# Performance work log

Hardware: AMD Instinct MI355X
Metric: run time of the kernel (lower is better)

The kernel has to match this reference:

```python
import jax, jax.numpy as jnp
import numpy as np

N_NODES = 300000
N_EDGES = 1200000
D = 128
B = 1000
VOCAB = 26  # vocab_size + 1


def setup_inputs() -> dict:
    key = jax.random.key(0)
    ks = jax.random.split(key, 10)
    x = jax.random.randint(ks[0], (N_NODES,), 0, VOCAB, dtype=jnp.int32)
    edge_index = jax.random.randint(ks[1], (2, N_EDGES), 0, N_NODES, dtype=jnp.int32)
    # cumulative protein boundaries: B proteins of equal length, last entry == N_NODES
    amino_acids_numbers = (jnp.arange(1, B + 1, dtype=jnp.int32) * (N_NODES // B))
    s = 1.0 / np.sqrt(D)
    emb = jax.random.normal(ks[2], (VOCAB, D), dtype=jnp.float32)
    W_rel1 = jax.random.uniform(ks[3], (D, D), jnp.float32, -s, s)
    b_rel1 = jax.random.uniform(ks[4], (D,), jnp.float32, -s, s)
    W_root1 = jax.random.uniform(ks[5], (D, D), jnp.float32, -s, s)
    W_rel2 = jax.random.uniform(ks[6], (D, D), jnp.float32, -s, s)
    b_rel2 = jax.random.uniform(ks[7], (D,), jnp.float32, -s, s)
    W_root2 = jax.random.uniform(ks[8], (D, D), jnp.float32, -s, s)
    return {"x": x, "edge_index": edge_index, "amino_acids_numbers": amino_acids_numbers,
            "emb": emb, "W_rel1": W_rel1, "b_rel1": b_rel1, "W_root1": W_root1,
            "W_rel2": W_rel2, "b_rel2": b_rel2, "W_root2": W_root2}


def _graph_conv(nodes, src, tgt, W_rel, b_rel, W_root, n):
    # PyG GraphConv (aggr='add'): out = Lin_rel(sum_{j->i} x_j) + Lin_root(x_i)
    agg = jax.ops.segment_sum(nodes[src], tgt, num_segments=n)  # [N, D]
    return agg @ W_rel.T + b_rel + nodes @ W_root.T


def reference(x, edge_index, amino_acids_numbers, emb,
              W_rel1, b_rel1, W_root1, W_rel2, b_rel2, W_root2):
    n = x.shape[0]
    src, tgt = edge_index[0], edge_index[1]
    nodes = emb[x]  # [N, D] embedding lookup
    nodes = _graph_conv(nodes, src, tgt, W_rel1, b_rel1, W_root1, n)
    nodes = _graph_conv(nodes, src, tgt, W_rel2, b_rel2, W_root2, n)
    # segment mean pooling over [start:end) slices defined by cumulative ends
    ends = amino_acids_numbers
    seg = jnp.searchsorted(ends, jnp.arange(n), side='right')  # node -> protein id
    b = ends.shape[0]
    sums = jax.ops.segment_sum(nodes, seg, num_segments=b)  # [B, D]
    counts = jnp.diff(ends, prepend=jnp.zeros((1,), ends.dtype)).astype(nodes.dtype)
    return sums / counts[:, None]
```

## Files before the change

kernel.cpp:

```cpp
#include <hip/hip_runtime.h>

#define DD 128
#define VV 26
#define NW 13
#define CS8 8
#define NB 256
#define TWIN 512

__device__ __forceinline__ unsigned wsum(unsigned v) {
#pragma unroll
    for (int m = 32; m >= 1; m >>= 1) v += __shfl_xor(v, m, 64);
    return v;
}

__device__ __forceinline__ int seg_guess(const int* ends, int B, int t, int Lavg) {
    int p = t / Lavg;
    if (p > B - 1) p = B - 1;
    while (p > 0 && ends[p - 1] > t) --p;
    while (ends[p] <= t) ++p;
    return p;
}

__device__ __forceinline__ int bseg(const int* cumx, int j) {
    int lo = 0, hi = NB - 1;
    while (lo < hi) {
        int mid = (lo + hi + 1) >> 1;
        if (cumx[mid] <= j) lo = mid; else hi = mid - 1;
    }
    return lo;
}

__global__ __launch_bounds__(1024)
void k_sort_pre(const int* __restrict__ src, const int* __restrict__ tgt,
                const int* __restrict__ x, const int* __restrict__ ends,
                int E, int B, int chunk, int chunkp, int Lavg,
                const float* __restrict__ emb,
                const float* __restrict__ W1r, const float* __restrict__ b1,
                const float* __restrict__ W1o,
                const float* __restrict__ W2r, const float* __restrict__ W2o,
                unsigned short* __restrict__ sorted_tl, unsigned* __restrict__ sorted_s,
                int* __restrict__ segstart, int* __restrict__ seghist,
                float* __restrict__ P1, float* __restrict__ P2,
                float* __restrict__ P3, float* __restrict__ uvec,
                float* __restrict__ wvec) {
    extern __shared__ int lds[];
    int tid = threadIdx.x;

    if (blockIdx.x >= NB) {
        float* e1r = (float*)lds;
        float* r1r = e1r + DD;
        float* b1s = r1r + DD;
        int v = blockIdx.x - NB;
        int d = tid;
        if (d < DD) {
            const float* e = emb + v * DD;
            const float* w1r = W1r + d * DD;
            const float* w1o = W1o + d * DD;
            float s1 = 0.f, s2 = 0.f;
            for (int k = 0; k < DD; ++k) {
                float ev = e[k];
                s1 += ev * w1r[k];
                s2 += ev * w1o[k];
            }
            e1r[d] = s1; r1r[d] = s2; b1s[d] = b1[d];
        }
        __syncthreads();
        if (d < DD) {
            const float* wr = W2r + d * DD;
            const float* wo = W2o + d * DD;
            float p1 = 0.f, p2 = 0.f, p3 = 0.f, su = 0.f, sw = 0.f;
            for (int k = 0; k < DD; ++k) {
                float a = wr[k], b = wo[k], ee = e1r[k], r = r1r[k], bb = b1s[k];
                p1 += ee * a; p2 += r * a + ee * b; p3 += r * b;
                su += bb * a; sw += bb * b;
            }
            P1[v * DD + d] = p1; P2[v * DD + d] = p2; P3[v * DD + d] = p3;
            if (v == 0) { uvec[d] = su; wvec[d] = sw; }
        }
        return;
    }

    int* lds_ends = lds;
    int* scan     = lds + B;
    int* cur      = scan + 1024;
    unsigned short* lpe = (unsigned short*)(cur + B);
    unsigned short* stl = lpe + chunkp;
    unsigned* sts = (unsigned*)(stl + chunkp);

    int b = blockIdx.x;
    int e0 = b * chunk;
    int e1 = min(E, e0 + chunk);
    int clen = e1 - e0;

    for (int i = tid; i < B; i += 1024) lds_ends[i] = ends[i];
    scan[tid] = 0;
    __syncthreads();

    for (int i = tid; i < clen; i += 1024) {
        int t = tgt[e0 + i];
        int p = seg_guess(lds_ends, B, t, Lavg);
        atomicAdd(&scan[p], 1);
        lpe[i] = (unsigned short)p;
    }
    __syncthreads();
    int v = scan[tid];
    if (tid < B) seghist[b * B + tid] = v;
    for (int off = 1; off < 1024; off <<= 1) {
        int t = (tid >= off) ? scan[tid - off] : 0;
        __syncthreads();
        scan[tid] += t;
        __syncthreads();
    }
    if (tid < B) {
        int excl = scan[tid] - v;
        cur[tid] = excl;
        segstart[b * B + tid] = e0 + excl;
    }
    __syncthreads();

    for (int i = tid; i < clen; i += 1024) {
        int e = e0 + i;
        int p = lpe[i];
        int s = src[e];
        int t = tgt[e];
        int lbl = x[s];
        int pst = (p == 0) ? 0 : lds_ends[p - 1];
        int pos = atomicAdd(&cur[p], 1);
        stl[pos] = (unsigned short)(((t - pst) << 5) | lbl);
        sts[pos] = (unsigned)s;
    }
    __syncthreads();

    for (int i = tid; i < clen; i += 1024) {
        sorted_tl[e0 + i] = stl[i];
        sorted_s[e0 + i] = sts[i];
    }
}

__global__ __launch_bounds__(256)
void k_counts(const int* __restrict__ x, const int* __restrict__ ends,
              const int* __restrict__ segstart, const int* __restrict__ seghist,
              int B, int E, const unsigned short* __restrict__ sorted_tl,
              unsigned* __restrict__ counts,
              float* __restrict__ CpG, float* __restrict__ HpG) {
    __shared__ unsigned tab[TWIN * CS8];
    __shared__ int sc[NB], cumx[NB + 1], segb[NB];
    __shared__ unsigned red[4][2 * NW];
    int p = blockIdx.x, tid = threadIdx.x;
    int start = (p == 0) ? 0 : ends[p - 1];
    int end = ends[p];
    int Lp = end - start;

    int h = seghist[tid * B + p];
    segb[tid] = segstart[tid * B + p];
    sc[tid] = h;
    __syncthreads();
    for (int off = 1; off < NB; off <<= 1) {
        int t = (tid >= off) ? sc[tid - off] : 0;
        __syncthreads();
        sc[tid] += t;
        __syncthreads();
    }
    cumx[tid] = sc[tid] - h;
    if (tid == NB - 1) cumx[NB] = sc[NB - 1];
    __syncthreads();
    int Dp = cumx[NB];

    unsigned cpw[NW], hpw[NW];
#pragma unroll
    for (int w = 0; w < NW; ++w) { cpw[w] = 0u; hpw[w] = 0u; }

    for (int i = start + tid; i < end; i += 256) {
        int l = x[i];
        unsigned inc = 1u << ((l & 1) * 16);
        int wi = l >> 1;
#pragma unroll
        for (int w = 0; w < NW; ++w) hpw[w] += (w == wi) ? inc : 0u;
    }

    for (int w0 = 0; w0 < Lp; w0 += TWIN) {
        int wlen = min(TWIN, Lp - w0);
        __syncthreads();
        for (int i = tid; i < wlen * CS8; i += 256) tab[i] = 0u;
        __syncthreads();
        for (int j = tid; j < Dp; j += 256) {
            int bb = bseg(cumx, j);
            int pos = segb[bb] + (j - cumx[bb]);
            unsigned tl = (unsigned)sorted_tl[pos];
            int lbl = (int)(tl & 31u);
            int tloc = (int)(tl >> 5) - w0;
            if ((unsigned)tloc < (unsigned)wlen)
                atomicAdd(&tab[tloc * CS8 + (lbl >> 2)], 1u << ((lbl & 3) * 8));
            if (w0 == 0) {
                unsigned inc = 1u << ((lbl & 1) * 16);
                int wi = lbl >> 1;
#pragma unroll
                for (int w = 0; w < NW; ++w) cpw[w] += (w == wi) ? inc : 0u;
            }
        }
        __syncthreads();
        for (int idx = tid; idx < wlen * CS8; idx += 256) {
            int r = idx >> 3, w = idx & 7;
            counts[((size_t)(start + w0 + r)) * CS8 + w] = tab[r * CS8 + w];
        }
    }

    int wave = tid >> 6, lane = tid & 63;
#pragma unroll
    for (int w = 0; w < NW; ++w) {
        unsigned a = wsum(cpw[w]); if (lane == 0) red[wave][w] = a;
        unsigned b = wsum(hpw[w]); if (lane == 0) red[wave][NW + w] = b;
    }
    __syncthreads();
    if (tid < 2 * NW) {
        unsigned t = red[0][tid] + red[1][tid] + red[2][tid] + red[3][tid];
        int grp = tid / NW, w = tid % NW;
        float* dst = (grp == 0) ? (CpG + (size_t)p * VV) : (HpG + (size_t)p * VV);
        dst[w * 2] = (float)(t & 0xFFFFu);
        if (w * 2 + 1 < VV) dst[w * 2 + 1] = (float)(t >> 16);
    }
}

__global__ __launch_bounds__(256)
void k_protein(const int* __restrict__ ends,
               const int* __restrict__ segstart, const int* __restrict__ seghist,
               const unsigned* __restrict__ sorted_s,
               const unsigned* __restrict__ counts,
               const float* __restrict__ CpG, const float* __restrict__ HpG,
               const float* __restrict__ P1, const float* __restrict__ P2,
               const float* __restrict__ P3, const float* __restrict__ uvec,
               const float* __restrict__ wvec, const float* __restrict__ b2,
               int B, int E, float* __restrict__ out) {
    __shared__ int sc[NB], cumx[NB + 1], segb[NB];
    __shared__ unsigned red[4][14];
    __shared__ float c2f[VV], cpf[VV], hpf[VV];
    int p = blockIdx.x, tid = threadIdx.x;
    int start = (p == 0) ? 0 : ends[p - 1];
    int end = ends[p];

    int h = seghist[tid * B + p];
    segb[tid] = segstart[tid * B + p];
    sc[tid] = h;
    __syncthreads();
    for (int off = 1; off < NB; off <<= 1) {
        int t = (tid >= off) ? sc[tid - off] : 0;
        __syncthreads();
        sc[tid] += t;
        __syncthreads();
    }
    cumx[tid] = sc[tid] - h;
    if (tid == NB - 1) cumx[NB] = sc[NB - 1];
    __syncthreads();
    int Dp = cumx[NB];

    unsigned ua[7], ub[7];
#pragma unroll
    for (int k = 0; k < 7; ++k) { ua[k] = 0u; ub[k] = 0u; }
    for (int j = tid; j < Dp; j += 256) {
        int bb = bseg(cumx, j);
        int pos = segb[bb] + (j - cumx[bb]);
        int s = (int)sorted_s[pos];
        const uint4* cb = reinterpret_cast<const uint4*>(counts + (size_t)s * CS8);
        uint4 c0 = cb[0], c1 = cb[1];
        unsigned w;
        w = c0.x; ua[0] += w & 0x00FF00FFu; ub[0] += (w >> 8) & 0x00FF00FFu;
        w = c0.y; ua[1] += w & 0x00FF00FFu; ub[1] += (w >> 8) & 0x00FF00FFu;
        w = c0.z; ua[2] += w & 0x00FF00FFu; ub[2] += (w >> 8) & 0x00FF00FFu;
        w = c0.w; ua[3] += w & 0x00FF00FFu; ub[3] += (w >> 8) & 0x00FF00FFu;
        w = c1.x; ua[4] += w & 0x00FF00FFu; ub[4] += (w >> 8) & 0x00FF00FFu;
        w = c1.y; ua[5] += w & 0x00FF00FFu; ub[5] += (w >> 8) & 0x00FF00FFu;
        w = c1.z; ua[6] += w & 0x00FF00FFu; ub[6] += (w >> 8) & 0x00FF00FFu;
    }

    int wave = tid >> 6, lane = tid & 63;
#pragma unroll
    for (int k = 0; k < 7; ++k) {
        unsigned a = wsum(ua[k]); if (lane == 0) red[wave][2 * k] = a;
        unsigned b = wsum(ub[k]); if (lane == 0) red[wave][2 * k + 1] = b;
    }
    if (tid >= 64 && tid < 64 + VV)   cpf[tid - 64]  = CpG[(size_t)p * VV + (tid - 64)];
    if (tid >= 128 && tid < 128 + VV) hpf[tid - 128] = HpG[(size_t)p * VV + (tid - 128)];
    __syncthreads();
    if (tid < 14) {
        unsigned t = red[0][tid] + red[1][tid] + red[2][tid] + red[3][tid];
        int k = tid >> 1, isB = tid & 1;
        int base = 4 * k + isB;
        c2f[base] = (float)(t & 0xFFFFu);
        if (base + 2 < VV) c2f[base + 2] = (float)(t >> 16);
    }
    __syncthreads();

    if (tid < DD) {
        int d = tid;
        float acc = 0.f;
#pragma unroll
        for (int v = 0; v < VV; ++v)
            acc += c2f[v] * P1[v * DD + d] + cpf[v] * P2[v * DD + d] + hpf[v] * P3[v * DD + d];
        float Lp = (float)(end - start);
        float invL = 1.f / Lp;
        float Dpf = (float)Dp;
        out[(size_t)p * DD + d] = acc * invL + (Dpf * invL) * uvec[d] + wvec[d] + b2[d];
    }
}

extern "C" void kernel_launch(void* const* d_in, const int* in_sizes, int n_in,
                              void* d_out, int out_size, void* d_ws, size_t ws_size,
                              hipStream_t stream) {
    const int*   x       = (const int*)d_in[0];
    const int*   edge    = (const int*)d_in[1];
    const int*   ends    = (const int*)d_in[2];
    const float* emb     = (const float*)d_in[3];
    const float* W_rel1  = (const float*)d_in[4];
    const float* b_rel1  = (const float*)d_in[5];
    const float* W_root1 = (const float*)d_in[6];
    const float* W_rel2  = (const float*)d_in[7];
    const float* b_rel2  = (const float*)d_in[8];
    const float* W_root2 = (const float*)d_in[9];

    const int N = in_sizes[0];
    const int E = in_sizes[1] / 2;
    const int B = in_sizes[2];
    const int Lavg = (N / B) > 0 ? (N / B) : 1;
    const int chunk = (E + NB - 1) / NB;
    const int chunkp = (chunk + 1) & ~1;

    const int* srcp = edge;
    const int* tgtp = edge + E;

    auto align256 = [](size_t v) { return (v + 255) & ~(size_t)255; };
    char* ws = (char*)d_ws;
    size_t off = 0;
    unsigned* counts = (unsigned*)(ws + off);               off += align256((size_t)N * CS8 * 4);
    int* segstart = (int*)(ws + off);                       off += align256((size_t)NB * B * 4);
    int* seghist = (int*)(ws + off);                        off += align256((size_t)NB * B * 4);
    unsigned short* sorted_tl = (unsigned short*)(ws + off); off += align256((size_t)E * 2);
    unsigned* sorted_s = (unsigned*)(ws + off);             off += align256((size_t)E * 4);
    float* CpG = (float*)(ws + off);                        off += align256((size_t)B * VV * 4);
    float* HpG = (float*)(ws + off);                        off += align256((size_t)B * VV * 4);
    float* P1 = (float*)(ws + off);                         off += align256((size_t)VV * DD * 4);
    float* P2 = (float*)(ws + off);                         off += align256((size_t)VV * DD * 4);
    float* P3 = (float*)(ws + off);                         off += align256((size_t)VV * DD * 4);
    float* uvec = (float*)(ws + off);                       off += align256((size_t)DD * 4);
    float* wvec = (float*)(ws + off);                       off += align256((size_t)DD * 4);
    (void)ws_size; (void)n_in; (void)out_size;


    size_t ldsb = (size_t)(B + 1024 + B) * 4 + (size_t)chunkp * 4 + (size_t)chunk * 4;
    k_sort_pre<<<NB + VV, 1024, ldsb, stream>>>(
        srcp, tgtp, x, ends, E, B, chunk, chunkp, Lavg,
        emb, W_rel1, b_rel1, W_root1, W_rel2, W_root2,
        sorted_tl, sorted_s, segstart, seghist, P1, P2, P3, uvec, wvec);

    k_counts<<<B, 256, 0, stream>>>(x, ends, segstart, seghist, B, E, sorted_tl,
                                    counts, CpG, HpG);

    k_protein<<<B, 256, 0, stream>>>(ends, segstart, seghist, sorted_s, counts, CpG, HpG,
                                     P1, P2, P3, uvec, wvec, b_rel2, B, E, (float*)d_out);
}
```

Before: 72.24 us.

## Merge three kernels into one cooperative persistent kernel with grid syncs

Replaces the sort, counts and protein kernels with a single cooperative kernel of 256 blocks of 1024 threads that separates phases with grid.sync. The per-protein prefix scan over chunk histograms is computed once into global buffers (pcum/psegb) and reused by both later phases, where before it was repeated in each kernel. Per-protein work now runs in 1024-thread blocks striding over proteins, so each block handles about four proteins. The aim is to remove launch gaps and redundant scans, at the cost of grid-barrier overhead, fewer resident blocks for the per-protein phases, and the 26 weight-precompute blocks now sitting serially in front of the sort in the first blocks.

```diff
diff --git a/kernel.cpp b/kernel.cpp
--- a/kernel.cpp
+++ b/kernel.cpp
@@ -1,11 +1,16 @@
 #include <hip/hip_runtime.h>
+#include <hip/hip_cooperative_groups.h>
+
+namespace cg = cooperative_groups;
 
 #define DD 128
 #define VV 26
 #define NW 13
 #define CS8 8
-#define NB 256
+#define G 256
+#define T 1024
 #define TWIN 512
+#define PCS 260
 
 __device__ __forceinline__ unsigned wsum(unsigned v) {
 #pragma unroll
@@ -22,7 +27,7 @@
 }
 
 __device__ __forceinline__ int bseg(const int* cumx, int j) {
-    int lo = 0, hi = NB - 1;
+    int lo = 0, hi = G - 1;
     while (lo < hi) {
         int mid = (lo + hi + 1) >> 1;
         if (cumx[mid] <= j) lo = mid; else hi = mid - 1;
@@ -30,38 +35,38 @@
     return lo;
 }
 
-__global__ __launch_bounds__(1024)
-void k_sort_pre(const int* __restrict__ src, const int* __restrict__ tgt,
-                const int* __restrict__ x, const int* __restrict__ ends,
-                int E, int B, int chunk, int chunkp, int Lavg,
-                const float* __restrict__ emb,
-                const float* __restrict__ W1r, const float* __restrict__ b1,
-                const float* __restrict__ W1o,
-                const float* __restrict__ W2r, const float* __restrict__ W2o,
-                unsigned short* __restrict__ sorted_tl, unsigned* __restrict__ sorted_s,
-                int* __restrict__ segstart, int* __restrict__ seghist,
-                float* __restrict__ P1, float* __restrict__ P2,
-                float* __restrict__ P3, float* __restrict__ uvec,
-                float* __restrict__ wvec) {
-    extern __shared__ int lds[];
+__global__ void __launch_bounds__(T, 4)
+k_all(const int* __restrict__ src, const int* __restrict__ tgt,
+      const int* __restrict__ x, const int* __restrict__ ends,
+      int E, int B, int chunk, int Lavg,
+      const float* __restrict__ emb, const float* __restrict__ W1r,
+      const float* __restrict__ b1, const float* __restrict__ W1o,
+      const float* __restrict__ W2r, const float* __restrict__ W2o,
+      int* __restrict__ segstart, int* __restrict__ seghist,
+      unsigned short* __restrict__ sorted_tl, unsigned* __restrict__ sorted_s,
+      int* __restrict__ pcum, int* __restrict__ psegb,
+      unsigned* __restrict__ counts, float* __restrict__ CpG, float* __restrict__ HpG,
+      float* __restrict__ P1, float* __restrict__ P2, float* __restrict__ P3,
+      float* __restrict__ uvec, float* __restrict__ wvec,
+      const float* __restrict__ b2, float* __restrict__ out)
+{
+    extern __shared__ char smem[];
+    cg::grid_group grid = cg::this_grid();
     int tid = threadIdx.x;
-
-    if (blockIdx.x >= NB) {
-        float* e1r = (float*)lds;
+    int blk = blockIdx.x;
+    int chunkp = (chunk + 1) & ~1;
+
+    if (blk < VV) {
+        float* e1r = (float*)smem;
         float* r1r = e1r + DD;
         float* b1s = r1r + DD;
-        int v = blockIdx.x - NB;
-        int d = tid;
+        int v = blk, d = tid;
         if (d < DD) {
             const float* e = emb + v * DD;
             const float* w1r = W1r + d * DD;
             const float* w1o = W1o + d * DD;
             float s1 = 0.f, s2 = 0.f;
-            for (int k = 0; k < DD; ++k) {
-                float ev = e[k];
-                s1 += ev * w1r[k];
-                s2 += ev * w1o[k];
-            }
+            for (int k = 0; k < DD; ++k) { float ev = e[k]; s1 += ev * w1r[k]; s2 += ev * w1o[k]; }
             e1r[d] = s1; r1r[d] = s2; b1s[d] = b1[d];
         }
         __syncthreads();
@@ -70,236 +75,236 @@
             const float* wo = W2o + d * DD;
             float p1 = 0.f, p2 = 0.f, p3 = 0.f, su = 0.f, sw = 0.f;
             for (int k = 0; k < DD; ++k) {
-                float a = wr[k], b = wo[k], ee = e1r[k], r = r1r[k], bb = b1s[k];
-                p1 += ee * a; p2 += r * a + ee * b; p3 += r * b;
-                su += bb * a; sw += bb * b;
+                float a = wr[k], bb = wo[k], ee = e1r[k], r = r1r[k], c = b1s[k];
+                p1 += ee * a; p2 += r * a + ee * bb; p3 += r * bb;
+                su += c * a; sw += c * bb;
             }
             P1[v * DD + d] = p1; P2[v * DD + d] = p2; P3[v * DD + d] = p3;
             if (v == 0) { uvec[d] = su; wvec[d] = sw; }
         }
-        return;
-    }
-
-    int* lds_ends = lds;
-    int* scan     = lds + B;
-    int* cur      = scan + 1024;
-    unsigned short* lpe = (unsigned short*)(cur + B);
-    unsigned short* stl = lpe + chunkp;
-    unsigned* sts = (unsigned*)(stl + chunkp);
-
-    int b = blockIdx.x;
-    int e0 = b * chunk;
-    int e1 = min(E, e0 + chunk);
-    int clen = e1 - e0;
-
-    for (int i = tid; i < B; i += 1024) lds_ends[i] = ends[i];
-    scan[tid] = 0;
-    __syncthreads();
-
-    for (int i = tid; i < clen; i += 1024) {
-        int t = tgt[e0 + i];
-        int p = seg_guess(lds_ends, B, t, Lavg);
-        atomicAdd(&scan[p], 1);
-        lpe[i] = (unsigned short)p;
-    }
-    __syncthreads();
-    int v = scan[tid];
-    if (tid < B) seghist[b * B + tid] = v;
-    for (int off = 1; off < 1024; off <<= 1) {
-        int t = (tid >= off) ? scan[tid - off] : 0;
-        __syncthreads();
-        scan[tid] += t;
-        __syncthreads();
-    }
-    if (tid < B) {
-        int excl = scan[tid] - v;
-        cur[tid] = excl;
-        segstart[b * B + tid] = e0 + excl;
-    }
-    __syncthreads();
-
-    for (int i = tid; i < clen; i += 1024) {
-        int e = e0 + i;
-        int p = lpe[i];
-        int s = src[e];
-        int t = tgt[e];
-        int lbl = x[s];
-        int pst = (p == 0) ? 0 : lds_ends[p - 1];
-        int pos = atomicAdd(&cur[p], 1);
-        stl[pos] = (unsigned short)(((t - pst) << 5) | lbl);
-        sts[pos] = (unsigned)s;
-    }
-    __syncthreads();
-
-    for (int i = tid; i < clen; i += 1024) {
-        sorted_tl[e0 + i] = stl[i];
-        sorted_s[e0 + i] = sts[i];
-    }
-}
-
-__global__ __launch_bounds__(256)
-void k_counts(const int* __restrict__ x, const int* __restrict__ ends,
-              const int* __restrict__ segstart, const int* __restrict__ seghist,
-              int B, int E, const unsigned short* __restrict__ sorted_tl,
-              unsigned* __restrict__ counts,
-              float* __restrict__ CpG, float* __restrict__ HpG) {
-    __shared__ unsigned tab[TWIN * CS8];
-    __shared__ int sc[NB], cumx[NB + 1], segb[NB];
-    __shared__ unsigned red[4][2 * NW];
-    int p = blockIdx.x, tid = threadIdx.x;
-    int start = (p == 0) ? 0 : ends[p - 1];
-    int end = ends[p];
-    int Lp = end - start;
-
-    int h = seghist[tid * B + p];
-    segb[tid] = segstart[tid * B + p];
-    sc[tid] = h;
-    __syncthreads();
-    for (int off = 1; off < NB; off <<= 1) {
-        int t = (tid >= off) ? sc[tid - off] : 0;
-        __syncthreads();
-        sc[tid] += t;
-        __syncthreads();
-    }
-    cumx[tid] = sc[tid] - h;
-    if (tid == NB - 1) cumx[NB] = sc[NB - 1];
-    __syncthreads();
-    int Dp = cumx[NB];
-
-    unsigned cpw[NW], hpw[NW];
-#pragma unroll
-    for (int w = 0; w < NW; ++w) { cpw[w] = 0u; hpw[w] = 0u; }
-
-    for (int i = start + tid; i < end; i += 256) {
-        int l = x[i];
-        unsigned inc = 1u << ((l & 1) * 16);
-        int wi = l >> 1;
-#pragma unroll
-        for (int w = 0; w < NW; ++w) hpw[w] += (w == wi) ? inc : 0u;
-    }
-
-    for (int w0 = 0; w0 < Lp; w0 += TWIN) {
-        int wlen = min(TWIN, Lp - w0);
-        __syncthreads();
-        for (int i = tid; i < wlen * CS8; i += 256) tab[i] = 0u;
-        __syncthreads();
-        for (int j = tid; j < Dp; j += 256) {
-            int bb = bseg(cumx, j);
-            int pos = segb[bb] + (j - cumx[bb]);
-            unsigned tl = (unsigned)sorted_tl[pos];
-            int lbl = (int)(tl & 31u);
-            int tloc = (int)(tl >> 5) - w0;
-            if ((unsigned)tloc < (unsigned)wlen)
-                atomicAdd(&tab[tloc * CS8 + (lbl >> 2)], 1u << ((lbl & 3) * 8));
-            if (w0 == 0) {
-                unsigned inc = 1u << ((lbl & 1) * 16);
-                int wi = lbl >> 1;
-#pragma unroll
-                for (int w = 0; w < NW; ++w) cpw[w] += (w == wi) ? inc : 0u;
-            }
-        }
-        __syncthreads();
-        for (int idx = tid; idx < wlen * CS8; idx += 256) {
-            int r = idx >> 3, w = idx & 7;
-            counts[((size_t)(start + w0 + r)) * CS8 + w] = tab[r * CS8 + w];
-        }
-    }
-
-    int wave = tid >> 6, lane = tid & 63;
-#pragma unroll
-    for (int w = 0; w < NW; ++w) {
-        unsigned a = wsum(cpw[w]); if (lane == 0) red[wave][w] = a;
-        unsigned b = wsum(hpw[w]); if (lane == 0) red[wave][NW + w] = b;
-    }
-    __syncthreads();
-    if (tid < 2 * NW) {
-        unsigned t = red[0][tid] + red[1][tid] + red[2][tid] + red[3][tid];
-        int grp = tid / NW, w = tid % NW;
-        float* dst = (grp == 0) ? (CpG + (size_t)p * VV) : (HpG + (size_t)p * VV);
-        dst[w * 2] = (float)(t & 0xFFFFu);
-        if (w * 2 + 1 < VV) dst[w * 2 + 1] = (float)(t >> 16);
-    }
-}
-
-__global__ __launch_bounds__(256)
-void k_protein(const int* __restrict__ ends,
-               const int* __restrict__ segstart, const int* __restrict__ seghist,
-               const unsigned* __restrict__ sorted_s,
-               const unsigned* __restrict__ counts,
-               const float* __restrict__ CpG, const float* __restrict__ HpG,
-               const float* __restrict__ P1, const float* __restrict__ P2,
-               const float* __restrict__ P3, const float* __restrict__ uvec,
-               const float* __restrict__ wvec, const float* __restrict__ b2,
-               int B, int E, float* __restrict__ out) {
-    __shared__ int sc[NB], cumx[NB + 1], segb[NB];
-    __shared__ unsigned red[4][14];
-    __shared__ float c2f[VV], cpf[VV], hpf[VV];
-    int p = blockIdx.x, tid = threadIdx.x;
-    int start = (p == 0) ? 0 : ends[p - 1];
-    int end = ends[p];
-
-    int h = seghist[tid * B + p];
-    segb[tid] = segstart[tid * B + p];
-    sc[tid] = h;
-    __syncthreads();
-    for (int off = 1; off < NB; off <<= 1) {
-        int t = (tid >= off) ? sc[tid - off] : 0;
-        __syncthreads();
-        sc[tid] += t;
-        __syncthreads();
-    }
-    cumx[tid] = sc[tid] - h;
-    if (tid == NB - 1) cumx[NB] = sc[NB - 1];
-    __syncthreads();
-    int Dp = cumx[NB];
-
-    unsigned ua[7], ub[7];
-#pragma unroll
-    for (int k = 0; k < 7; ++k) { ua[k] = 0u; ub[k] = 0u; }
-    for (int j = tid; j < Dp; j += 256) {
-        int bb = bseg(cumx, j);
-        int pos = segb[bb] + (j - cumx[bb]);
-        int s = (int)sorted_s[pos];
-        const uint4* cb = reinterpret_cast<const uint4*>(counts + (size_t)s * CS8);
-        uint4 c0 = cb[0], c1 = cb[1];
-        unsigned w;
-        w = c0.x; ua[0] += w & 0x00FF00FFu; ub[0] += (w >> 8) & 0x00FF00FFu;
-        w = c0.y; ua[1] += w & 0x00FF00FFu; ub[1] += (w >> 8) & 0x00FF00FFu;
-        w = c0.z; ua[2] += w & 0x00FF00FFu; ub[2] += (w >> 8) & 0x00FF00FFu;
-        w = c0.w; ua[3] += w & 0x00FF00FFu; ub[3] += (w >> 8) & 0x00FF00FFu;
-        w = c1.x; ua[4] += w & 0x00FF00FFu; ub[4] += (w >> 8) & 0x00FF00FFu;
-        w = c1.y; ua[5] += w & 0x00FF00FFu; ub[5] += (w >> 8) & 0x00FF00FFu;
-        w = c1.z; ua[6] += w & 0x00FF00FFu; ub[6] += (w >> 8) & 0x00FF00FFu;
-    }
-
-    int wave = tid >> 6, lane = tid & 63;
-#pragma unroll
-    for (int k = 0; k < 7; ++k) {
-        unsigned a = wsum(ua[k]); if (lane == 0) red[wave][2 * k] = a;
-        unsigned b = wsum(ub[k]); if (lane == 0) red[wave][2 * k + 1] = b;
-    }
-    if (tid >= 64 && tid < 64 + VV)   cpf[tid - 64]  = CpG[(size_t)p * VV + (tid - 64)];
-    if (tid >= 128 && tid < 128 + VV) hpf[tid - 128] = HpG[(size_t)p * VV + (tid - 128)];
-    __syncthreads();
-    if (tid < 14) {
-        unsigned t = red[0][tid] + red[1][tid] + red[2][tid] + red[3][tid];
-        int k = tid >> 1, isB = tid & 1;
-        int base = 4 * k + isB;
-        c2f[base] = (float)(t & 0xFFFFu);
-        if (base + 2 < VV) c2f[base + 2] = (float)(t >> 16);
-    }
-    __syncthreads();
-
-    if (tid < DD) {
-        int d = tid;
-        float acc = 0.f;
-#pragma unroll
-        for (int v = 0; v < VV; ++v)
-            acc += c2f[v] * P1[v * DD + d] + cpf[v] * P2[v * DD + d] + hpf[v] * P3[v * DD + d];
-        float Lp = (float)(end - start);
-        float invL = 1.f / Lp;
-        float Dpf = (float)Dp;
-        out[(size_t)p * DD + d] = acc * invL + (Dpf * invL) * uvec[d] + wvec[d] + b2[d];
+        __syncthreads();
+    }
+
+    {
+        int* lds_ends = (int*)smem;
+        int* scan = lds_ends + 1024;
+        int* cur = scan + 1024;
+        unsigned short* lpe = (unsigned short*)(cur + 1024);
+        unsigned short* stl = lpe + chunkp;
+        unsigned* sts = (unsigned*)(stl + chunkp);
+
+        int e0 = blk * chunk;
+        int e1 = min(E, e0 + chunk);
+        int clen = e1 - e0;
+        for (int i = tid; i < B; i += T) lds_ends[i] = ends[i];
+        scan[tid] = 0;
+        __syncthreads();
+        for (int i = tid; i < clen; i += T) {
+            int t = tgt[e0 + i];
+            int p = seg_guess(lds_ends, B, t, Lavg);
+            atomicAdd(&scan[p], 1);
+            lpe[i] = (unsigned short)p;
+        }
+        __syncthreads();
+        int v = scan[tid];
+        if (tid < B) seghist[blk * B + tid] = v;
+        for (int off = 1; off < T; off <<= 1) {
+            int t = (tid >= off) ? scan[tid - off] : 0;
+            __syncthreads();
+            scan[tid] += t;
+            __syncthreads();
+        }
+        if (tid < B) {
+            int excl = scan[tid] - v;
+            cur[tid] = excl;
+            segstart[blk * B + tid] = e0 + excl;
+        }
+        __syncthreads();
+        for (int i = tid; i < clen; i += T) {
+            int e = e0 + i;
+            int p = lpe[i];
+            int s = src[e];
+            int t = tgt[e];
+            int lbl = x[s];
+            int pst = (p == 0) ? 0 : lds_ends[p - 1];
+            int pos = atomicAdd(&cur[p], 1);
+            stl[pos] = (unsigned short)(((t - pst) << 5) | lbl);
+            sts[pos] = (unsigned)s;
+        }
+        __syncthreads();
+        for (int i = tid; i < clen; i += T) {
+            sorted_tl[e0 + i] = stl[i];
+            sorted_s[e0 + i] = sts[i];
+        }
+    }
+
+    grid.sync();
+
+    {
+        int* h = (int*)smem;
+        for (int p = blk; p < B; p += G) {
+            int v = 0;
+            if (tid < G) { v = seghist[tid * B + p]; h[tid] = v; }
+            __syncthreads();
+            for (int off = 1; off < G; off <<= 1) {
+                int t = (tid >= off && tid < G) ? h[tid - off] : 0;
+                __syncthreads();
+                if (tid < G) h[tid] += t;
+                __syncthreads();
+            }
+            if (tid < G) {
+                pcum[p * PCS + tid] = h[tid] - v;
+                psegb[p * G + tid] = segstart[tid * B + p];
+            }
+            if (tid == G - 1) pcum[p * PCS + G] = h[G - 1];
+            __syncthreads();
+        }
+    }
+
+    grid.sync();
+
+    {
+        unsigned* tab = (unsigned*)smem;
+        int* cumx = (int*)(smem + TWIN * CS8 * 4);
+        int* segb = cumx + 260;
+        unsigned* red = (unsigned*)(segb + 256);
+
+        for (int p = blk; p < B; p += G) {
+            int start = (p == 0) ? 0 : ends[p - 1];
+            int end = ends[p];
+            int Lp = end - start;
+            if (tid <= G) cumx[tid] = pcum[p * PCS + tid];
+            if (tid < G) segb[tid] = psegb[p * G + tid];
+            __syncthreads();
+            int Dp = cumx[G];
+
+            unsigned cpw[NW], hpw[NW];
+#pragma unroll
+            for (int w = 0; w < NW; ++w) { cpw[w] = 0u; hpw[w] = 0u; }
+
+            for (int i = start + tid; i < end; i += T) {
+                int l = x[i];
+                unsigned inc = 1u << ((l & 1) * 16);
+                int wi = l >> 1;
+#pragma unroll
+                for (int w = 0; w < NW; ++w) hpw[w] += (w == wi) ? inc : 0u;
+            }
+
+            for (int w0 = 0; w0 < Lp; w0 += TWIN) {
+                int wlen = min(TWIN, Lp - w0);
+                __syncthreads();
+                for (int i = tid; i < wlen * CS8; i += T) tab[i] = 0u;
+                __syncthreads();
+                for (int j = tid; j < Dp; j += T) {
+                    int bb = bseg(cumx, j);
+                    int pos = segb[bb] + (j - cumx[bb]);
+                    unsigned tl = (unsigned)sorted_tl[pos];
+                    int lbl = (int)(tl & 31u);
+                    int tloc = (int)(tl >> 5) - w0;
+                    if ((unsigned)tloc < (unsigned)wlen)
+                        atomicAdd(&tab[tloc * CS8 + (lbl >> 2)], 1u << ((lbl & 3) * 8));
+                    if (w0 == 0) {
+                        unsigned inc = 1u << ((lbl & 1) * 16);
+                        int wi = lbl >> 1;
+#pragma unroll
+                        for (int w = 0; w < NW; ++w) cpw[w] += (w == wi) ? inc : 0u;
+                    }
+                }
+                __syncthreads();
+                for (int idx = tid; idx < wlen * CS8; idx += T) {
+                    int r = idx >> 3, w = idx & 7;
+                    counts[((size_t)(start + w0 + r)) * CS8 + w] = tab[r * CS8 + w];
+                }
+            }
+
+            int wave = tid >> 6, lane = tid & 63;
+#pragma unroll
+            for (int w = 0; w < NW; ++w) {
+                unsigned a = wsum(cpw[w]); if (lane == 0) red[wave * 26 + w] = a;
+                unsigned b = wsum(hpw[w]); if (lane == 0) red[wave * 26 + NW + w] = b;
+            }
+            __syncthreads();
+            if (tid < 2 * NW) {
+                unsigned t = 0;
+#pragma unroll
+                for (int w = 0; w < 16; ++w) t += red[w * 26 + tid];
+                int grp = tid / NW, w = tid % NW;
+                float* dst = (grp == 0) ? (CpG + (size_t)p * VV) : (HpG + (size_t)p * VV);
+                dst[w * 2] = (float)(t & 0xFFFFu);
+                if (w * 2 + 1 < VV) dst[w * 2 + 1] = (float)(t >> 16);
+            }
+            __syncthreads();
+        }
+    }
+
+    grid.sync();
+
+    {
+        int* cumx = (int*)smem;
+        int* segb = cumx + 260;
+        unsigned* red = (unsigned*)(segb + 256);
+        float* c2f = (float*)(red + 16 * 14);
+        float* cpf = c2f + VV;
+        float* hpf = cpf + VV;
+
+        for (int p = blk; p < B; p += G) {
+            int start = (p == 0) ? 0 : ends[p - 1];
+            int end = ends[p];
+            if (tid <= G) cumx[tid] = pcum[p * PCS + tid];
+            if (tid < G) segb[tid] = psegb[p * G + tid];
+            __syncthreads();
+            int Dp = cumx[G];
+
+            unsigned ua[7], ub[7];
+#pragma unroll
+            for (int k = 0; k < 7; ++k) { ua[k] = 0u; ub[k] = 0u; }
+            for (int j = tid; j < Dp; j += T) {
+                int bb = bseg(cumx, j);
+                int pos = segb[bb] + (j - cumx[bb]);
+                int s = (int)sorted_s[pos];
+                const uint4* cb = reinterpret_cast<const uint4*>(counts + (size_t)s * CS8);
+                uint4 c0 = cb[0], c1 = cb[1];
+                unsigned w;
+                w = c0.x; ua[0] += w & 0x00FF00FFu; ub[0] += (w >> 8) & 0x00FF00FFu;
+                w = c0.y; ua[1] += w & 0x00FF00FFu; ub[1] += (w >> 8) & 0x00FF00FFu;
+                w = c0.z; ua[2] += w & 0x00FF00FFu; ub[2] += (w >> 8) & 0x00FF00FFu;
+                w = c0.w; ua[3] += w & 0x00FF00FFu; ub[3] += (w >> 8) & 0x00FF00FFu;
+                w = c1.x; ua[4] += w & 0x00FF00FFu; ub[4] += (w >> 8) & 0x00FF00FFu;
+                w = c1.y; ua[5] += w & 0x00FF00FFu; ub[5] += (w >> 8) & 0x00FF00FFu;
+                w = c1.z; ua[6] += w & 0x00FF00FFu; ub[6] += (w >> 8) & 0x00FF00FFu;
+            }
+
+            int wave = tid >> 6, lane = tid & 63;
+#pragma unroll
+            for (int k = 0; k < 7; ++k) {
+                unsigned a = wsum(ua[k]); if (lane == 0) red[wave * 14 + 2 * k] = a;
+                unsigned b = wsum(ub[k]); if (lane == 0) red[wave * 14 + 2 * k + 1] = b;
+            }
+            if (tid >= 64 && tid < 64 + VV)   cpf[tid - 64]  = CpG[(size_t)p * VV + (tid - 64)];
+            if (tid >= 128 && tid < 128 + VV) hpf[tid - 128] = HpG[(size_t)p * VV + (tid - 128)];
+            __syncthreads();
+            if (tid < 14) {
+                unsigned t = 0;
+#pragma unroll
+                for (int w = 0; w < 16; ++w) t += red[w * 14 + tid];
+                int k = tid >> 1, isB = tid & 1;
+                int base = 4 * k + isB;
+                c2f[base] = (float)(t & 0xFFFFu);
+                if (base + 2 < VV) c2f[base + 2] = (float)(t >> 16);
+            }
+            __syncthreads();
+            if (tid < DD) {
+                int d = tid;
+                float acc = 0.f;
+#pragma unroll
+                for (int v = 0; v < VV; ++v)
+                    acc += c2f[v] * P1[v * DD + d] + cpf[v] * P2[v * DD + d] + hpf[v] * P3[v * DD + d];
+                float Lpf = (float)(end - start);
+                float invL = 1.f / Lpf;
+                out[(size_t)p * DD + d] = acc * invL + ((float)Dp * invL) * uvec[d] + wvec[d] + b2[d];
+            }
+            __syncthreads();
+        }
     }
 }
 
@@ -317,12 +322,12 @@
     const float* b_rel2  = (const float*)d_in[8];
     const float* W_root2 = (const float*)d_in[9];
 
-    const int N = in_sizes[0];
-    const int E = in_sizes[1] / 2;
-    const int B = in_sizes[2];
-    const int Lavg = (N / B) > 0 ? (N / B) : 1;
-    const int chunk = (E + NB - 1) / NB;
-    const int chunkp = (chunk + 1) & ~1;
+    int N = in_sizes[0];
+    int E = in_sizes[1] / 2;
+    int B = in_sizes[2];
+    int Lavg = (N / B) > 0 ? (N / B) : 1;
+    int chunk = (E + G - 1) / G;
+    int chunkp = (chunk + 1) & ~1;
 
     const int* srcp = edge;
     const int* tgtp = edge + E;
@@ -330,30 +335,38 @@
     auto align256 = [](size_t v) { return (v + 255) & ~(size_t)255; };
     char* ws = (char*)d_ws;
     size_t off = 0;
-    unsigned* counts = (unsigned*)(ws + off);               off += align256((size_t)N * CS8 * 4);
-    int* segstart = (int*)(ws + off);                       off += align256((size_t)NB * B * 4);
-    int* seghist = (int*)(ws + off);                        off += align256((size_t)NB * B * 4);
+    unsigned* counts = (unsigned*)(ws + off);                off += align256((size_t)N * CS8 * 4);
+    int* segstart = (int*)(ws + off);                        off += align256((size_t)G * B * 4);
+    int* seghist = (int*)(ws + off);                         off += align256((size_t)G * B * 4);
     unsigned short* sorted_tl = (unsigned short*)(ws + off); off += align256((size_t)E * 2);
-    unsigned* sorted_s = (unsigned*)(ws + off);             off += align256((size_t)E * 4);
-    float* CpG = (float*)(ws + off);                        off += align256((size_t)B * VV * 4);
-    float* HpG = (float*)(ws + off);                        off += align256((size_t)B * VV * 4);
-    float* P1 = (float*)(ws + off);                         off += align256((size_t)VV * DD * 4);
-    float* P2 = (float*)(ws + off);                         off += align256((size_t)VV * DD * 4);
-    float* P3 = (float*)(ws + off);                         off += align256((size_t)VV * DD * 4);
-    float* uvec = (float*)(ws + off);                       off += align256((size_t)DD * 4);
-    float* wvec = (float*)(ws + off);                       off += align256((size_t)DD * 4);
+    unsigned* sorted_s = (unsigned*)(ws + off);              off += align256((size_t)E * 4);
+    int* pcum = (int*)(ws + off);                            off += align256((size_t)B * PCS * 4);
+    int* psegb = (int*)(ws + off);                           off += align256((size_t)B * G * 4);
+    float* CpG = (float*)(ws + off);                         off += align256((size_t)B * VV * 4);
+    float* HpG = (float*)(ws + off);                         off += align256((size_t)B * VV * 4);
+    float* P1 = (float*)(ws + off);                          off += align256((size_t)VV * DD * 4);
+    float* P2 = (float*)(ws + off);                          off += align256((size_t)VV * DD * 4);
+    float* P3 = (float*)(ws + off);                          off += align256((size_t)VV * DD * 4);
+    float* uvec = (float*)(ws + off);                        off += align256((size_t)DD * 4);
+    float* wvec = (float*)(ws + off);                        off += align256((size_t)DD * 4);
     (void)ws_size; (void)n_in; (void)out_size;
 
-
-    size_t ldsb = (size_t)(B + 1024 + B) * 4 + (size_t)chunkp * 4 + (size_t)chunk * 4;
-    k_sort_pre<<<NB + VV, 1024, ldsb, stream>>>(
-        srcp, tgtp, x, ends, E, B, chunk, chunkp, Lavg,
-        emb, W_rel1, b_rel1, W_root1, W_rel2, W_root2,
-        sorted_tl, sorted_s, segstart, seghist, P1, P2, P3, uvec, wvec);
-
-    k_counts<<<B, 256, 0, stream>>>(x, ends, segstart, seghist, B, E, sorted_tl,
-                                    counts, CpG, HpG);
-
-    k_protein<<<B, 256, 0, stream>>>(ends, segstart, seghist, sorted_s, counts, CpG, HpG,
-                                     P1, P2, P3, uvec, wvec, b_rel2, B, E, (float*)d_out);
-}
+    float* outp = (float*)d_out;
+
+
+    size_t ldsb = (size_t)3 * 1024 * 4 + (size_t)chunkp * 4 + (size_t)chunk * 4;
+
+    void* args[] = {
+        (void*)&srcp, (void*)&tgtp, (void*)&x, (void*)&ends,
+        (void*)&E, (void*)&B, (void*)&chunk, (void*)&Lavg,
+        (void*)&emb, (void*)&W_rel1, (void*)&b_rel1, (void*)&W_root1,
+        (void*)&W_rel2, (void*)&W_root2,
+        (void*)&segstart, (void*)&seghist, (void*)&sorted_tl, (void*)&sorted_s,
+        (void*)&pcum, (void*)&psegb,
+        (void*)&counts, (void*)&CpG, (void*)&HpG,
+        (void*)&P1, (void*)&P2, (void*)&P3, (void*)&uvec, (void*)&wvec,
+        (void*)&b_rel2, (void*)&outp
+    };
+    hipLaunchCooperativeKernel((const void*)k_all, dim3(G), dim3(T), args,
+                               (unsigned)ldsb, stream);
+}
```

New measurement: 269.1 us. 273% more time.

## Replace LDS Hillis-Steele scans with wave shuffles and transpose segment tables

Applied to the files above, without the earlier changes.

The block-wide prefix scans in the sort and per-protein kernels are rewritten as wave-level shuffle scans plus a small cross-wave offset, which removes many __syncthreads rounds. A new transpose kernel converts the per-chunk segment histogram and start tables into protein-major layout, so the per-protein kernels read contiguous rows instead of strided columns. This adds an extra kernel launch and extra workspace buffers.

```diff
diff --git a/kernel.cpp b/kernel.cpp
--- a/kernel.cpp
+++ b/kernel.cpp
@@ -4,12 +4,22 @@
 #define VV 26
 #define NW 13
 #define CS8 8
-#define NB 256
+#define G 256
 #define TWIN 512
 
 __device__ __forceinline__ unsigned wsum(unsigned v) {
 #pragma unroll
     for (int m = 32; m >= 1; m >>= 1) v += __shfl_xor(v, m, 64);
+    return v;
+}
+
+__device__ __forceinline__ int wscan_incl(int v) {
+    int lane = threadIdx.x & 63;
+#pragma unroll
+    for (int off = 1; off < 64; off <<= 1) {
+        int t = __shfl_up(v, off, 64);
+        if (lane >= off) v += t;
+    }
     return v;
 }
 
@@ -22,7 +32,7 @@
 }
 
 __device__ __forceinline__ int bseg(const int* cumx, int j) {
-    int lo = 0, hi = NB - 1;
+    int lo = 0, hi = G - 1;
     while (lo < hi) {
         int mid = (lo + hi + 1) >> 1;
         if (cumx[mid] <= j) lo = mid; else hi = mid - 1;
@@ -33,7 +43,7 @@
 __global__ __launch_bounds__(1024)
 void k_sort_pre(const int* __restrict__ src, const int* __restrict__ tgt,
                 const int* __restrict__ x, const int* __restrict__ ends,
-                int E, int B, int chunk, int chunkp, int Lavg,
+                int E, int B, int chunk, int Lavg,
                 const float* __restrict__ emb,
                 const float* __restrict__ W1r, const float* __restrict__ b1,
                 const float* __restrict__ W1o,
@@ -45,23 +55,20 @@
                 float* __restrict__ wvec) {
     extern __shared__ int lds[];
     int tid = threadIdx.x;
-
-    if (blockIdx.x >= NB) {
+    int chunkp = (chunk + 1) & ~1;
+
+    if (blockIdx.x >= G) {
         float* e1r = (float*)lds;
         float* r1r = e1r + DD;
         float* b1s = r1r + DD;
-        int v = blockIdx.x - NB;
+        int v = blockIdx.x - G;
         int d = tid;
         if (d < DD) {
             const float* e = emb + v * DD;
             const float* w1r = W1r + d * DD;
             const float* w1o = W1o + d * DD;
             float s1 = 0.f, s2 = 0.f;
-            for (int k = 0; k < DD; ++k) {
-                float ev = e[k];
-                s1 += ev * w1r[k];
-                s2 += ev * w1o[k];
-            }
+            for (int k = 0; k < DD; ++k) { float ev = e[k]; s1 += ev * w1r[k]; s2 += ev * w1o[k]; }
             e1r[d] = s1; r1r[d] = s2; b1s[d] = b1[d];
         }
         __syncthreads();
@@ -70,9 +77,9 @@
             const float* wo = W2o + d * DD;
             float p1 = 0.f, p2 = 0.f, p3 = 0.f, su = 0.f, sw = 0.f;
             for (int k = 0; k < DD; ++k) {
-                float a = wr[k], b = wo[k], ee = e1r[k], r = r1r[k], bb = b1s[k];
-                p1 += ee * a; p2 += r * a + ee * b; p3 += r * b;
-                su += bb * a; sw += bb * b;
+                float a = wr[k], bb = wo[k], ee = e1r[k], r = r1r[k], c = b1s[k];
+                p1 += ee * a; p2 += r * a + ee * bb; p3 += r * bb;
+                su += c * a; sw += c * bb;
             }
             P1[v * DD + d] = p1; P2[v * DD + d] = p2; P3[v * DD + d] = p3;
             if (v == 0) { uvec[d] = su; wvec[d] = sw; }
@@ -81,9 +88,10 @@
     }
 
     int* lds_ends = lds;
-    int* scan     = lds + B;
-    int* cur      = scan + 1024;
-    unsigned short* lpe = (unsigned short*)(cur + B);
+    int* hist = lds_ends + 1024;
+    int* cur = hist + 1024;
+    int* wsums = cur + 1024;
+    unsigned short* lpe = (unsigned short*)(wsums + 16);
     unsigned short* stl = lpe + chunkp;
     unsigned* sts = (unsigned*)(stl + chunkp);
 
@@ -93,26 +101,27 @@
     int clen = e1 - e0;
 
     for (int i = tid; i < B; i += 1024) lds_ends[i] = ends[i];
-    scan[tid] = 0;
+    hist[tid] = 0;
     __syncthreads();
 
     for (int i = tid; i < clen; i += 1024) {
         int t = tgt[e0 + i];
         int p = seg_guess(lds_ends, B, t, Lavg);
-        atomicAdd(&scan[p], 1);
+        atomicAdd(&hist[p], 1);
         lpe[i] = (unsigned short)p;
     }
     __syncthreads();
-    int v = scan[tid];
+
+    int v = hist[tid];
     if (tid < B) seghist[b * B + tid] = v;
-    for (int off = 1; off < 1024; off <<= 1) {
-        int t = (tid >= off) ? scan[tid - off] : 0;
-        __syncthreads();
-        scan[tid] += t;
-        __syncthreads();
-    }
+    int wave = tid >> 6, lane = tid & 63;
+    int incl = wscan_incl(v);
+    if (lane == 63) wsums[wave] = incl;
+    __syncthreads();
+    int offw = 0;
+    for (int w = 0; w < wave; ++w) offw += wsums[w];
+    int excl = incl + offw - v;
     if (tid < B) {
-        int excl = scan[tid] - v;
         cur[tid] = excl;
         segstart[b * B + tid] = e0 + excl;
     }
@@ -138,33 +147,49 @@
 }
 
 __global__ __launch_bounds__(256)
+void k_trans(const int* __restrict__ a, const int* __restrict__ c, int B,
+             int* __restrict__ aT, int* __restrict__ cT) {
+    __shared__ int ta[32][33], tc[32][33];
+    int b0 = blockIdx.x * 32;
+    int p0 = blockIdx.y * 32;
+    int tx = threadIdx.x & 31, ty = threadIdx.x >> 5;
+    for (int r = ty; r < 32; r += 8) {
+        int bb = b0 + r, pp = p0 + tx;
+        if (pp < B) { ta[r][tx] = a[bb * B + pp]; tc[r][tx] = c[bb * B + pp]; }
+    }
+    __syncthreads();
+    for (int r = ty; r < 32; r += 8) {
+        int pp = p0 + r, bb = b0 + tx;
+        if (pp < B) { aT[pp * G + bb] = ta[tx][r]; cT[pp * G + bb] = tc[tx][r]; }
+    }
+}
+
+__global__ __launch_bounds__(256)
 void k_counts(const int* __restrict__ x, const int* __restrict__ ends,
-              const int* __restrict__ segstart, const int* __restrict__ seghist,
+              const int* __restrict__ seghistT, const int* __restrict__ segstartT,
               int B, int E, const unsigned short* __restrict__ sorted_tl,
               unsigned* __restrict__ counts,
               float* __restrict__ CpG, float* __restrict__ HpG) {
     __shared__ unsigned tab[TWIN * CS8];
-    __shared__ int sc[NB], cumx[NB + 1], segb[NB];
+    __shared__ int cumx[G + 4], segb[G], wsums[4];
     __shared__ unsigned red[4][2 * NW];
     int p = blockIdx.x, tid = threadIdx.x;
+    int wave = tid >> 6, lane = tid & 63;
     int start = (p == 0) ? 0 : ends[p - 1];
     int end = ends[p];
     int Lp = end - start;
 
-    int h = seghist[tid * B + p];
-    segb[tid] = segstart[tid * B + p];
-    sc[tid] = h;
-    __syncthreads();
-    for (int off = 1; off < NB; off <<= 1) {
-        int t = (tid >= off) ? sc[tid - off] : 0;
-        __syncthreads();
-        sc[tid] += t;
-        __syncthreads();
-    }
-    cumx[tid] = sc[tid] - h;
-    if (tid == NB - 1) cumx[NB] = sc[NB - 1];
-    __syncthreads();
-    int Dp = cumx[NB];
+    int h = seghistT[p * G + tid];
+    segb[tid] = segstartT[p * G + tid];
+    int incl = wscan_incl(h);
+    if (lane == 63) wsums[wave] = incl;
+    __syncthreads();
+    int offw = 0;
+    for (int w = 0; w < wave; ++w) offw += wsums[w];
+    cumx[tid] = incl + offw - h;
+    if (tid == 255) cumx[G] = incl + offw;
+    __syncthreads();
+    int Dp = cumx[G];
 
     unsigned cpw[NW], hpw[NW];
 #pragma unroll
@@ -205,7 +230,6 @@
         }
     }
 
-    int wave = tid >> 6, lane = tid & 63;
 #pragma unroll
     for (int w = 0; w < NW; ++w) {
         unsigned a = wsum(cpw[w]); if (lane == 0) red[wave][w] = a;
@@ -223,7 +247,7 @@
 
 __global__ __launch_bounds__(256)
 void k_protein(const int* __restrict__ ends,
-               const int* __restrict__ segstart, const int* __restrict__ seghist,
+               const int* __restrict__ seghistT, const int* __restrict__ segstartT,
                const unsigned* __restrict__ sorted_s,
                const unsigned* __restrict__ counts,
                const float* __restrict__ CpG, const float* __restrict__ HpG,
@@ -231,27 +255,25 @@
                const float* __restrict__ P3, const float* __restrict__ uvec,
                const float* __restrict__ wvec, const float* __restrict__ b2,
                int B, int E, float* __restrict__ out) {
-    __shared__ int sc[NB], cumx[NB + 1], segb[NB];
+    __shared__ int cumx[G + 4], segb[G], wsums[4];
     __shared__ unsigned red[4][14];
     __shared__ float c2f[VV], cpf[VV], hpf[VV];
     int p = blockIdx.x, tid = threadIdx.x;
+    int wave = tid >> 6, lane = tid & 63;
     int start = (p == 0) ? 0 : ends[p - 1];
     int end = ends[p];
 
-    int h = seghist[tid * B + p];
-    segb[tid] = segstart[tid * B + p];
-    sc[tid] = h;
-    __syncthreads();
-    for (int off = 1; off < NB; off <<= 1) {
-        int t = (tid >= off) ? sc[tid - off] : 0;
-        __syncthreads();
-        sc[tid] += t;
-        __syncthreads();
-    }
-    cumx[tid] = sc[tid] - h;
-    if (tid == NB - 1) cumx[NB] = sc[NB - 1];
-    __syncthreads();
-    int Dp = cumx[NB];
+    int h = seghistT[p * G + tid];
+    segb[tid] = segstartT[p * G + tid];
+    int incl = wscan_incl(h);
+    if (lane == 63) wsums[wave] = incl;
+    __syncthreads();
+    int offw = 0;
+    for (int w = 0; w < wave; ++w) offw += wsums[w];
+    cumx[tid] = incl + offw - h;
+    if (tid == 255) cumx[G] = incl + offw;
+    __syncthreads();
+    int Dp = cumx[G];
 
     unsigned ua[7], ub[7];
 #pragma unroll
@@ -272,7 +294,6 @@
         w = c1.z; ua[6] += w & 0x00FF00FFu; ub[6] += (w >> 8) & 0x00FF00FFu;
     }
 
-    int wave = tid >> 6, lane = tid & 63;
 #pragma unroll
     for (int k = 0; k < 7; ++k) {
         unsigned a = wsum(ua[k]); if (lane == 0) red[wave][2 * k] = a;
@@ -321,7 +342,7 @@
     const int E = in_sizes[1] / 2;
     const int B = in_sizes[2];
     const int Lavg = (N / B) > 0 ? (N / B) : 1;
-    const int chunk = (E + NB - 1) / NB;
+    const int chunk = (E + G - 1) / G;
     const int chunkp = (chunk + 1) & ~1;
 
     const int* srcp = edge;
@@ -330,30 +351,35 @@
     auto align256 = [](size_t v) { return (v + 255) & ~(size_t)255; };
     char* ws = (char*)d_ws;
     size_t off = 0;
-    unsigned* counts = (unsigned*)(ws + off);               off += align256((size_t)N * CS8 * 4);
-    int* segstart = (int*)(ws + off);                       off += align256((size_t)NB * B * 4);
-    int* seghist = (int*)(ws + off);                        off += align256((size_t)NB * B * 4);
+    unsigned* counts = (unsigned*)(ws + off);                off += align256((size_t)N * CS8 * 4);
+    int* segstart = (int*)(ws + off);                        off += align256((size_t)G * B * 4);
+    int* seghist = (int*)(ws + off);                         off += align256((size_t)G * B * 4);
+    int* segstartT = (int*)(ws + off);                       off += align256((size_t)B * G * 4);
+    int* seghistT = (int*)(ws + off);                        off += align256((size_t)B * G * 4);
     unsigned short* sorted_tl = (unsigned short*)(ws + off); off += align256((size_t)E * 2);
-    unsigned* sorted_s = (unsigned*)(ws + off);             off += align256((size_t)E * 4);
-    float* CpG = (float*)(ws + off);                        off += align256((size_t)B * VV * 4);
-    float* HpG = (float*)(ws + off);                        off += align256((size_t)B * VV * 4);
-    float* P1 = (float*)(ws + off);                         off += align256((size_t)VV * DD * 4);
-    float* P2 = (float*)(ws + off);                         off += align256((size_t)VV * DD * 4);
-    float* P3 = (float*)(ws + off);                         off += align256((size_t)VV * DD * 4);
-    float* uvec = (float*)(ws + off);                       off += align256((size_t)DD * 4);
-    float* wvec = (float*)(ws + off);                       off += align256((size_t)DD * 4);
+    unsigned* sorted_s = (unsigned*)(ws + off);              off += align256((size_t)E * 4);
+    float* CpG = (float*)(ws + off);                         off += align256((size_t)B * VV * 4);
+    float* HpG = (float*)(ws + off);                         off += align256((size_t)B * VV * 4);
+    float* P1 = (float*)(ws + off);                          off += align256((size_t)VV * DD * 4);
+    float* P2 = (float*)(ws + off);                          off += align256((size_t)VV * DD * 4);
+    float* P3 = (float*)(ws + off);                          off += align256((size_t)VV * DD * 4);
+    float* uvec = (float*)(ws + off);                        off += align256((size_t)DD * 4);
+    float* wvec = (float*)(ws + off);                        off += align256((size_t)DD * 4);
     (void)ws_size; (void)n_in; (void)out_size;
 
 
-    size_t ldsb = (size_t)(B + 1024 + B) * 4 + (size_t)chunkp * 4 + (size_t)chunk * 4;
-    k_sort_pre<<<NB + VV, 1024, ldsb, stream>>>(
-        srcp, tgtp, x, ends, E, B, chunk, chunkp, Lavg,
+    size_t ldsb = (size_t)(3 * 1024 + 16) * 4 + (size_t)chunkp * 4 + (size_t)chunk * 4;
+    k_sort_pre<<<G + VV, 1024, ldsb, stream>>>(
+        srcp, tgtp, x, ends, E, B, chunk, Lavg,
         emb, W_rel1, b_rel1, W_root1, W_rel2, W_root2,
         sorted_tl, sorted_s, segstart, seghist, P1, P2, P3, uvec, wvec);
 
-    k_counts<<<B, 256, 0, stream>>>(x, ends, segstart, seghist, B, E, sorted_tl,
+    dim3 tgrid(G / 32, (B + 31) / 32);
+    k_trans<<<tgrid, 256, 0, stream>>>(seghist, segstart, B, seghistT, segstartT);
+
+    k_counts<<<B, 256, 0, stream>>>(x, ends, seghistT, segstartT, B, E, sorted_tl,
                                     counts, CpG, HpG);
 
-    k_protein<<<B, 256, 0, stream>>>(ends, segstart, seghist, sorted_s, counts, CpG, HpG,
+    k_protein<<<B, 256, 0, stream>>>(ends, seghistT, segstartT, sorted_s, counts, CpG, HpG,
                                      P1, P2, P3, uvec, wvec, b_rel2, B, E, (float*)d_out);
 }
```

Measured after the change: 70.93 us. No clear change (-1.8%).
